# Performance work log

Hardware: AMD Instinct MI355X
Metric: run time of the kernel (lower is better)

## Reference

```python
import jax, jax.numpy as jnp
import numpy as np

N_NODES = 100000
N_EDGES = 400000
D_FEAT = 128
HIDDEN = 64
BETA = 1.0  # temperature default in concrete_sample


def setup_inputs() -> dict:
    key = jax.random.key(0)
    k = jax.random.split(key, 6)
    embed = jax.random.normal(k[0], (N_NODES, D_FEAT), dtype=jnp.float32)
    # elayers: Linear(4*F, 64) -> ReLU -> Linear(64, 1)
    W1 = jax.random.normal(k[1], (4 * D_FEAT, HIDDEN), dtype=jnp.float32) * (1.0 / np.sqrt(4 * D_FEAT))
    b1 = jnp.zeros((HIDDEN,), dtype=jnp.float32)
    W2 = jax.random.normal(k[2], (HIDDEN, 1), dtype=jnp.float32) * (1.0 / np.sqrt(HIDDEN))
    b2 = jnp.zeros((1,), dtype=jnp.float32)
    # per-edge uniform noise, as in torch.rand(w.size()); keep away from {0,1}
    noise = jax.random.uniform(k[3], (N_EDGES,), dtype=jnp.float32, minval=1e-6, maxval=1.0 - 1e-6)
    col = jax.random.randint(k[4], (N_EDGES,), 0, N_NODES, dtype=jnp.int64 if jax.config.jax_enable_x64 else jnp.int32)
    row = jax.random.randint(k[5], (N_EDGES,), 0, N_NODES, dtype=jnp.int64 if jax.config.jax_enable_x64 else jnp.int32)
    return {"embed": embed, "W1": W1, "b1": b1, "W2": W2, "b2": b2,
            "noise": noise, "col": col, "row": row, "src_idx": 0, "dst_idx": 1}


def reference(embed, W1, b1, W2, b2, noise, col, row, src_idx, dst_idx):
    E = col.shape[0]
    F = embed.shape[1]
    # gather per-edge endpoint embeddings + broadcast explained src/dst embeddings
    col_emb = embed[col]                                    # [E, F]
    row_emb = embed[row]                                    # [E, F]
    src_emb = jnp.broadcast_to(embed[src_idx], (E, F))       # [E, F]
    dst_emb = jnp.broadcast_to(embed[dst_idx], (E, F))       # [E, F]
    emb = jnp.concatenate([col_emb, row_emb, src_emb, dst_emb], axis=-1)  # [E, 4F]
    # elayers MLP
    h = jax.nn.relu(emb @ W1 + b1)                          # [E, 64]
    w = (h @ W2 + b2).reshape(-1)                           # [E]
    # concrete_sample (training=True, sample_bias=0): logit(noise) + w, sigmoid
    gate_inputs = (jnp.log(noise) - jnp.log1p(-noise) + w) / BETA
    values = jax.nn.sigmoid(gate_inputs)                    # [E] edge mask
    return values
```

## Files before the change

### kernel.cpp

```cpp
#include <hip/hip_runtime.h>
#include <hip/hip_bf16.h>


typedef __bf16 bf16x8 __attribute__((ext_vector_type(8)));
typedef float  f32x16 __attribute__((ext_vector_type(16)));
typedef unsigned short u16;

#define WSTR 264
#define Z16 {0.f,0.f,0.f,0.f,0.f,0.f,0.f,0.f,0.f,0.f,0.f,0.f,0.f,0.f,0.f,0.f}

__device__ __forceinline__ unsigned bfbits(float f){
  unsigned u = __builtin_bit_cast(unsigned, f);
  return (u + 0x7fffu + ((u >> 16) & 1u)) >> 16;
}
__device__ __forceinline__ unsigned pk2(float a, float b){
  return bfbits(a) | (bfbits(b) << 16);
}
__device__ __forceinline__ float bflo(unsigned u){ return __builtin_bit_cast(float, u << 16); }
__device__ __forceinline__ float bfhi(unsigned u){ return __builtin_bit_cast(float, u & 0xffff0000u); }

__global__ __launch_bounds__(256, 3) void fg_kernel(
    const float* __restrict__ embed, const float* __restrict__ W1,
    const float* __restrict__ b1, const int* __restrict__ srcp,
    const int* __restrict__ dstp, u16* __restrict__ F, u16* __restrict__ G, int NN)
{
  __shared__ __align__(16) u16 sW[64 * WSTR];
  __shared__ float sC[64];
  __shared__ float sRed[256];
  int tid = threadIdx.x;

  #pragma unroll
  for (int i = 0; i < 16; ++i){
    int idx = i * 256 + tid;
    int k = idx >> 4, q = idx & 15;
    float4 v = *(const float4*)(W1 + k * 64 + q * 4);
    sW[(4*q+0) * WSTR + k] = (u16)bfbits(v.x);
    sW[(4*q+1) * WSTR + k] = (u16)bfbits(v.y);
    sW[(4*q+2) * WSTR + k] = (u16)bfbits(v.z);
    sW[(4*q+3) * WSTR + k] = (u16)bfbits(v.w);
  }
  {
    int h = tid & 63, part = tid >> 6;
    int si = srcp[0], di = dstp[0];
    const float* se  = embed + (size_t)si * 128 + part * 32;
    const float* de  = embed + (size_t)di * 128 + part * 32;
    const float* w1s = W1 + (256 + part * 32) * 64 + h;
    const float* w1d = W1 + (384 + part * 32) * 64 + h;
    float acc = 0.f;
    #pragma unroll 8
    for (int k = 0; k < 32; ++k){
      acc += se[k] * w1s[k * 64];
      acc += de[k] * w1d[k * 64];
    }
    sRed[tid] = acc;
  }
  __syncthreads();
  if (tid < 64) sC[tid] = b1[tid] + sRed[tid] + sRed[64+tid] + sRed[128+tid] + sRed[192+tid];
  __syncthreads();

  int lane = tid & 63, wave = tid >> 6;
  int nl = lane & 31, h5 = lane >> 5;
  int tile = blockIdx.x * 128 + wave * 32;
  if (tile >= NN) return;
  const float* erow = embed + (size_t)(tile + nl) * 128;
  f32x16 aF0 = Z16, aF1 = Z16, aG0 = Z16, aG1 = Z16;
  const u16* sw0 = sW + nl * WSTR;
  const u16* sw1 = sW + (32 + nl) * WSTR;
  #pragma unroll
  for (int s = 0; s < 8; ++s){
    int ko = s * 16 + h5 * 8;
    float4 x = *(const float4*)(erow + ko);
    float4 y = *(const float4*)(erow + ko + 4);
    uint4 u; u.x = pk2(x.x,x.y); u.y = pk2(x.z,x.w); u.z = pk2(y.x,y.y); u.w = pk2(y.z,y.w);
    bf16x8 a = __builtin_bit_cast(bf16x8, u);
    bf16x8 bF0 = *(const bf16x8*)(sw0 + ko);
    bf16x8 bF1 = *(const bf16x8*)(sw1 + ko);
    bf16x8 bG0 = *(const bf16x8*)(sw0 + 128 + ko);
    bf16x8 bG1 = *(const bf16x8*)(sw1 + 128 + ko);
    aF0 = __builtin_amdgcn_mfma_f32_32x32x16_bf16(a, bF0, aF0, 0, 0, 0);
    aF1 = __builtin_amdgcn_mfma_f32_32x32x16_bf16(a, bF1, aF1, 0, 0, 0);
    aG0 = __builtin_amdgcn_mfma_f32_32x32x16_bf16(a, bG0, aG0, 0, 0, 0);
    aG1 = __builtin_amdgcn_mfma_f32_32x32x16_bf16(a, bG1, aG1, 0, 0, 0);
  }
  float cv0 = sC[nl], cv1 = sC[32 + nl];
  #pragma unroll
  for (int r = 0; r < 16; ++r){
    int node = tile + (r & 3) + 8 * (r >> 2) + 4 * h5;
    u16* fr = F + (size_t)node * 64 + nl;
    u16* gr = G + (size_t)node * 64 + nl;
    fr[0]  = (u16)bfbits(aF0[r] + cv0);
    fr[32] = (u16)bfbits(aF1[r] + cv1);
    gr[0]  = (u16)bfbits(aG0[r]);
    gr[32] = (u16)bfbits(aG1[r]);
  }
}

__global__ __launch_bounds__(256, 8) void edge_kernel(
    const u16* __restrict__ F, const u16* __restrict__ G,
    const float* __restrict__ W2, const float* __restrict__ b2,
    const float* __restrict__ noise, const int* __restrict__ col,
    const int* __restrict__ row, float* __restrict__ out, int E)
{
  int tid = threadIdx.x;
  int lane = tid & 63, wave = tid >> 6;
  int j = lane & 7, grp = lane >> 3;
  int e0 = blockIdx.x * 32 + wave * 8;
  if (e0 >= E) return;
  int e = e0 + grp; if (e >= E) e = E - 1;
  int ci = col[e], ri = row[e];
  uint4 fv = ((const uint4*)(F + (size_t)ci * 64))[j];
  uint4 gv = ((const uint4*)(G + (size_t)ri * 64))[j];
  float4 w2a = ((const float4*)W2)[2 * j];
  float4 w2b = ((const float4*)W2)[2 * j + 1];
  float p = 0.f, h;
  h = fmaxf(bflo(fv.x) + bflo(gv.x), 0.f); p += h * w2a.x;
  h = fmaxf(bfhi(fv.x) + bfhi(gv.x), 0.f); p += h * w2a.y;
  h = fmaxf(bflo(fv.y) + bflo(gv.y), 0.f); p += h * w2a.z;
  h = fmaxf(bfhi(fv.y) + bfhi(gv.y), 0.f); p += h * w2a.w;
  h = fmaxf(bflo(fv.z) + bflo(gv.z), 0.f); p += h * w2b.x;
  h = fmaxf(bfhi(fv.z) + bfhi(gv.z), 0.f); p += h * w2b.y;
  h = fmaxf(bflo(fv.w) + bflo(gv.w), 0.f); p += h * w2b.z;
  h = fmaxf(bfhi(fv.w) + bfhi(gv.w), 0.f); p += h * w2b.w;
  p += __shfl_xor(p, 1, 64);
  p += __shfl_xor(p, 2, 64);
  p += __shfl_xor(p, 4, 64);
  if (j == 0 && e0 + grp < E){
    float ns = noise[e];
    float g = logf(ns) - log1pf(-ns) + p + b2[0];
    out[e] = 1.f / (1.f + expf(-g));
  }
}

__global__ void naive_kernel(const float* __restrict__ embed, const float* __restrict__ W1,
    const float* __restrict__ b1, const float* __restrict__ W2, const float* __restrict__ b2,
    const float* __restrict__ noise, const int* __restrict__ col, const int* __restrict__ row,
    const int* __restrict__ srcp, const int* __restrict__ dstp, float* __restrict__ out, int E)
{
  int e = blockIdx.x * 256 + threadIdx.x;
  if (e >= E) return;
  int ci = col[e], ri = row[e], si = srcp[0], di = dstp[0];
  const float* ce = embed + (size_t)ci * 128;
  const float* re = embed + (size_t)ri * 128;
  const float* se = embed + (size_t)si * 128;
  const float* de = embed + (size_t)di * 128;
  float w = b2[0];
  for (int jj = 0; jj < 64; ++jj){
    float hh = b1[jj];
    for (int k = 0; k < 128; ++k){
      hh += ce[k] * W1[k * 64 + jj] + re[k] * W1[(128 + k) * 64 + jj]
          + se[k] * W1[(256 + k) * 64 + jj] + de[k] * W1[(384 + k) * 64 + jj];
    }
    w += fmaxf(hh, 0.f) * W2[jj];
  }
  float ns = noise[e];
  float g = logf(ns) - log1pf(-ns) + w;
  out[e] = 1.f / (1.f + expf(-g));
}

extern "C" void kernel_launch(void* const* d_in, const int* in_sizes, int n_in,
                              void* d_out, int out_size, void* d_ws, size_t ws_size,
                              hipStream_t stream)
{
  const float* embed = (const float*)d_in[0];
  const float* W1    = (const float*)d_in[1];
  const float* b1    = (const float*)d_in[2];
  const float* W2    = (const float*)d_in[3];
  const float* b2    = (const float*)d_in[4];
  const float* noise = (const float*)d_in[5];
  const int*   col   = (const int*)d_in[6];
  const int*   rowp  = (const int*)d_in[7];
  const int*   srcp  = (const int*)d_in[8];
  const int*   dstp  = (const int*)d_in[9];
  const int E  = in_sizes[5];
  const int NN = in_sizes[0] / 128;
  float* out = (float*)d_out;

  const size_t fBytes = (size_t)NN * 64 * sizeof(u16);
  if (ws_size >= 2 * fBytes){
    u16* F = (u16*)d_ws;
    u16* G = (u16*)((char*)d_ws + fBytes);
    fg_kernel<<<(NN + 127) / 128, 256, 0, stream>>>(embed, W1, b1, srcp, dstp, F, G, NN);
    edge_kernel<<<(E + 31) / 32, 256, 0, stream>>>(F, G, W2, b2, noise, col, rowp, out, E);
  } else {
    naive_kernel<<<(E + 255) / 256, 256, 0, stream>>>(embed, W1, b1, W2, b2, noise,
                                                      col, rowp, srcp, dstp, out, E);
  }
}
```

Baseline: 134.0 us.

## Fuse node projection and edge scoring into one cooperative persistent kernel

Merges the per-node projection kernel and the per-edge scoring kernel into a single persistent cooperative kernel, with a grid-wide sync between the two phases. Blocks loop over node tiles and then over edges, and each wave now handles two edges per iteration to raise memory-level parallelism. This removes one kernel launch and its gap. In exchange it adds grid-sync overhead, adds host-side occupancy queries on every call, and limits the edge phase to the occupancy chosen for the heavier projection kernel.

```diff
diff --git a/kernel.cpp b/kernel.cpp
--- a/kernel.cpp
+++ b/kernel.cpp
@@ -1,6 +1,9 @@
 #include <hip/hip_runtime.h>
 #include <hip/hip_bf16.h>
-
+#include <hip/hip_cooperative_groups.h>
+
+
+namespace cg = cooperative_groups;
 
 typedef __bf16 bf16x8 __attribute__((ext_vector_type(8)));
 typedef float  f32x16 __attribute__((ext_vector_type(16)));
@@ -19,15 +22,33 @@
 __device__ __forceinline__ float bflo(unsigned u){ return __builtin_bit_cast(float, u << 16); }
 __device__ __forceinline__ float bfhi(unsigned u){ return __builtin_bit_cast(float, u & 0xffff0000u); }
 
-__global__ __launch_bounds__(256, 3) void fg_kernel(
+__device__ __forceinline__ float edge_dot(uint4 fv, uint4 gv, float4 w2a, float4 w2b){
+  float p = 0.f, h;
+  h = fmaxf(bflo(fv.x) + bflo(gv.x), 0.f); p += h * w2a.x;
+  h = fmaxf(bfhi(fv.x) + bfhi(gv.x), 0.f); p += h * w2a.y;
+  h = fmaxf(bflo(fv.y) + bflo(gv.y), 0.f); p += h * w2a.z;
+  h = fmaxf(bfhi(fv.y) + bfhi(gv.y), 0.f); p += h * w2a.w;
+  h = fmaxf(bflo(fv.z) + bflo(gv.z), 0.f); p += h * w2b.x;
+  h = fmaxf(bfhi(fv.z) + bfhi(gv.z), 0.f); p += h * w2b.y;
+  h = fmaxf(bflo(fv.w) + bflo(gv.w), 0.f); p += h * w2b.z;
+  h = fmaxf(bfhi(fv.w) + bfhi(gv.w), 0.f); p += h * w2b.w;
+  return p;
+}
+
+__global__ __launch_bounds__(256, 3) void fused_kernel(
     const float* __restrict__ embed, const float* __restrict__ W1,
     const float* __restrict__ b1, const int* __restrict__ srcp,
-    const int* __restrict__ dstp, u16* __restrict__ F, u16* __restrict__ G, int NN)
+    const int* __restrict__ dstp, const float* __restrict__ W2,
+    const float* __restrict__ b2, const float* __restrict__ noise,
+    const int* __restrict__ col, const int* __restrict__ row,
+    u16* __restrict__ F, u16* __restrict__ G, float* __restrict__ out,
+    int NN, int E, int nBlocks)
 {
   __shared__ __align__(16) u16 sW[64 * WSTR];
   __shared__ float sC[64];
   __shared__ float sRed[256];
   int tid = threadIdx.x;
+  int lane = tid & 63, wave = tid >> 6;
 
   #pragma unroll
   for (int i = 0; i < 16; ++i){
@@ -58,76 +79,82 @@
   if (tid < 64) sC[tid] = b1[tid] + sRed[tid] + sRed[64+tid] + sRed[128+tid] + sRed[192+tid];
   __syncthreads();
 
-  int lane = tid & 63, wave = tid >> 6;
   int nl = lane & 31, h5 = lane >> 5;
-  int tile = blockIdx.x * 128 + wave * 32;
-  if (tile >= NN) return;
-  const float* erow = embed + (size_t)(tile + nl) * 128;
-  f32x16 aF0 = Z16, aF1 = Z16, aG0 = Z16, aG1 = Z16;
   const u16* sw0 = sW + nl * WSTR;
   const u16* sw1 = sW + (32 + nl) * WSTR;
-  #pragma unroll
-  for (int s = 0; s < 8; ++s){
-    int ko = s * 16 + h5 * 8;
-    float4 x = *(const float4*)(erow + ko);
-    float4 y = *(const float4*)(erow + ko + 4);
-    uint4 u; u.x = pk2(x.x,x.y); u.y = pk2(x.z,x.w); u.z = pk2(y.x,y.y); u.w = pk2(y.z,y.w);
-    bf16x8 a = __builtin_bit_cast(bf16x8, u);
-    bf16x8 bF0 = *(const bf16x8*)(sw0 + ko);
-    bf16x8 bF1 = *(const bf16x8*)(sw1 + ko);
-    bf16x8 bG0 = *(const bf16x8*)(sw0 + 128 + ko);
-    bf16x8 bG1 = *(const bf16x8*)(sw1 + 128 + ko);
-    aF0 = __builtin_amdgcn_mfma_f32_32x32x16_bf16(a, bF0, aF0, 0, 0, 0);
-    aF1 = __builtin_amdgcn_mfma_f32_32x32x16_bf16(a, bF1, aF1, 0, 0, 0);
-    aG0 = __builtin_amdgcn_mfma_f32_32x32x16_bf16(a, bG0, aG0, 0, 0, 0);
-    aG1 = __builtin_amdgcn_mfma_f32_32x32x16_bf16(a, bG1, aG1, 0, 0, 0);
-  }
   float cv0 = sC[nl], cv1 = sC[32 + nl];
-  #pragma unroll
-  for (int r = 0; r < 16; ++r){
-    int node = tile + (r & 3) + 8 * (r >> 2) + 4 * h5;
-    u16* fr = F + (size_t)node * 64 + nl;
-    u16* gr = G + (size_t)node * 64 + nl;
-    fr[0]  = (u16)bfbits(aF0[r] + cv0);
-    fr[32] = (u16)bfbits(aF1[r] + cv1);
-    gr[0]  = (u16)bfbits(aG0[r]);
-    gr[32] = (u16)bfbits(aG1[r]);
-  }
-}
-
-__global__ __launch_bounds__(256, 8) void edge_kernel(
-    const u16* __restrict__ F, const u16* __restrict__ G,
-    const float* __restrict__ W2, const float* __restrict__ b2,
-    const float* __restrict__ noise, const int* __restrict__ col,
-    const int* __restrict__ row, float* __restrict__ out, int E)
-{
-  int tid = threadIdx.x;
-  int lane = tid & 63, wave = tid >> 6;
+  for (int tile0 = blockIdx.x * 128; tile0 < NN; tile0 += nBlocks * 128){
+    int tile = tile0 + wave * 32;
+    if (tile < NN){
+      const float* erow = embed + (size_t)(tile + nl) * 128;
+      f32x16 aF0 = Z16, aF1 = Z16, aG0 = Z16, aG1 = Z16;
+      #pragma unroll
+      for (int s = 0; s < 8; ++s){
+        int ko = s * 16 + h5 * 8;
+        float4 x = *(const float4*)(erow + ko);
+        float4 y = *(const float4*)(erow + ko + 4);
+        uint4 u; u.x = pk2(x.x,x.y); u.y = pk2(x.z,x.w); u.z = pk2(y.x,y.y); u.w = pk2(y.z,y.w);
+        bf16x8 a = __builtin_bit_cast(bf16x8, u);
+        bf16x8 bF0 = *(const bf16x8*)(sw0 + ko);
+        bf16x8 bF1 = *(const bf16x8*)(sw1 + ko);
+        bf16x8 bG0 = *(const bf16x8*)(sw0 + 128 + ko);
+        bf16x8 bG1 = *(const bf16x8*)(sw1 + 128 + ko);
+        aF0 = __builtin_amdgcn_mfma_f32_32x32x16_bf16(a, bF0, aF0, 0, 0, 0);
+        aF1 = __builtin_amdgcn_mfma_f32_32x32x16_bf16(a, bF1, aF1, 0, 0, 0);
+        aG0 = __builtin_amdgcn_mfma_f32_32x32x16_bf16(a, bG0, aG0, 0, 0, 0);
+        aG1 = __builtin_amdgcn_mfma_f32_32x32x16_bf16(a, bG1, aG1, 0, 0, 0);
+      }
+      #pragma unroll
+      for (int r = 0; r < 16; ++r){
+        int node = tile + (r & 3) + 8 * (r >> 2) + 4 * h5;
+        u16* fr = F + (size_t)node * 64 + nl;
+        u16* gr = G + (size_t)node * 64 + nl;
+        fr[0]  = (u16)bfbits(aF0[r] + cv0);
+        fr[32] = (u16)bfbits(aF1[r] + cv1);
+        gr[0]  = (u16)bfbits(aG0[r]);
+        gr[32] = (u16)bfbits(aG1[r]);
+      }
+    }
+  }
+
+  __threadfence();
+  cg::this_grid().sync();
+  __threadfence();
+
   int j = lane & 7, grp = lane >> 3;
-  int e0 = blockIdx.x * 32 + wave * 8;
-  if (e0 >= E) return;
-  int e = e0 + grp; if (e >= E) e = E - 1;
-  int ci = col[e], ri = row[e];
-  uint4 fv = ((const uint4*)(F + (size_t)ci * 64))[j];
-  uint4 gv = ((const uint4*)(G + (size_t)ri * 64))[j];
   float4 w2a = ((const float4*)W2)[2 * j];
   float4 w2b = ((const float4*)W2)[2 * j + 1];
-  float p = 0.f, h;
-  h = fmaxf(bflo(fv.x) + bflo(gv.x), 0.f); p += h * w2a.x;
-  h = fmaxf(bfhi(fv.x) + bfhi(gv.x), 0.f); p += h * w2a.y;
-  h = fmaxf(bflo(fv.y) + bflo(gv.y), 0.f); p += h * w2a.z;
-  h = fmaxf(bfhi(fv.y) + bfhi(gv.y), 0.f); p += h * w2a.w;
-  h = fmaxf(bflo(fv.z) + bflo(gv.z), 0.f); p += h * w2b.x;
-  h = fmaxf(bfhi(fv.z) + bfhi(gv.z), 0.f); p += h * w2b.y;
-  h = fmaxf(bflo(fv.w) + bflo(gv.w), 0.f); p += h * w2b.z;
-  h = fmaxf(bfhi(fv.w) + bfhi(gv.w), 0.f); p += h * w2b.w;
-  p += __shfl_xor(p, 1, 64);
-  p += __shfl_xor(p, 2, 64);
-  p += __shfl_xor(p, 4, 64);
-  if (j == 0 && e0 + grp < E){
-    float ns = noise[e];
-    float g = logf(ns) - log1pf(-ns) + p + b2[0];
-    out[e] = 1.f / (1.f + expf(-g));
+  float b2v = b2[0];
+  int wgid = blockIdx.x * 4 + wave;
+  int stride = nBlocks * 4 * 16;
+  for (int base = wgid * 16; base < E; base += stride){
+    int eA = base + grp;
+    int eB = base + 8 + grp;
+    int eAc = eA < E ? eA : E - 1;
+    int eBc = eB < E ? eB : E - 1;
+    int ciA = col[eAc], riA = row[eAc];
+    int ciB = col[eBc], riB = row[eBc];
+    uint4 fvA = ((const uint4*)(F + (size_t)ciA * 64))[j];
+    uint4 gvA = ((const uint4*)(G + (size_t)riA * 64))[j];
+    uint4 fvB = ((const uint4*)(F + (size_t)ciB * 64))[j];
+    uint4 gvB = ((const uint4*)(G + (size_t)riB * 64))[j];
+    float pA = edge_dot(fvA, gvA, w2a, w2b);
+    float pB = edge_dot(fvB, gvB, w2a, w2b);
+    pA += __shfl_xor(pA, 1, 64); pB += __shfl_xor(pB, 1, 64);
+    pA += __shfl_xor(pA, 2, 64); pB += __shfl_xor(pB, 2, 64);
+    pA += __shfl_xor(pA, 4, 64); pB += __shfl_xor(pB, 4, 64);
+    if (j == 0){
+      if (eA < E){
+        float ns = noise[eA];
+        float g = logf(ns) - log1pf(-ns) + pA + b2v;
+        out[eA] = 1.f / (1.f + expf(-g));
+      }
+      if (eB < E){
+        float ns = noise[eB];
+        float g = logf(ns) - log1pf(-ns) + pB + b2v;
+        out[eB] = 1.f / (1.f + expf(-g));
+      }
+    }
   }
 }
 
@@ -171,16 +198,29 @@
   const int*   rowp  = (const int*)d_in[7];
   const int*   srcp  = (const int*)d_in[8];
   const int*   dstp  = (const int*)d_in[9];
-  const int E  = in_sizes[5];
-  const int NN = in_sizes[0] / 128;
+  int E  = in_sizes[5];
+  int NN = in_sizes[0] / 128;
   float* out = (float*)d_out;
 
   const size_t fBytes = (size_t)NN * 64 * sizeof(u16);
   if (ws_size >= 2 * fBytes){
     u16* F = (u16*)d_ws;
     u16* G = (u16*)((char*)d_ws + fBytes);
-    fg_kernel<<<(NN + 127) / 128, 256, 0, stream>>>(embed, W1, b1, srcp, dstp, F, G, NN);
-    edge_kernel<<<(E + 31) / 32, 256, 0, stream>>>(F, G, W2, b2, noise, col, rowp, out, E);
+    int dev = 0; hipGetDevice(&dev);
+    int nCU = 256;
+    hipDeviceGetAttribute(&nCU, hipDeviceAttributeMultiprocessorCount, dev);
+    int occ = 1;
+    hipOccupancyMaxActiveBlocksPerMultiprocessor(&occ, fused_kernel, 256, 0);
+    if (occ < 1) occ = 1;
+    int nBlocks = nCU * occ;
+    int maxUseful = (NN + 127) / 128;
+    if (nBlocks > maxUseful) nBlocks = maxUseful;
+    void* args[] = { (void*)&embed, (void*)&W1, (void*)&b1, (void*)&srcp, (void*)&dstp,
+                     (void*)&W2, (void*)&b2, (void*)&noise, (void*)&col, (void*)&rowp,
+                     (void*)&F, (void*)&G, (void*)&out, (void*)&NN, (void*)&E,
+                     (void*)&nBlocks };
+    hipLaunchCooperativeKernel((const void*)fused_kernel, dim3(nBlocks), dim3(256),
+                               args, 0, stream);
   } else {
     naive_kernel<<<(E + 255) / 256, 256, 0, stream>>>(embed, W1, b1, W2, b2, noise,
                                                       col, rowp, srcp, dstp, out, E);
```

Measured after the change: 315.2 us. 2.35x slower.

## Process one edge per thread in edge kernel and raise fg occupancy bound

Applied to the files above, without the earlier changes.

The edge kernel changes from eight lanes per edge with a shuffle reduction to one thread per edge. Each thread loads the full 128-byte F and G rows as eight uint4 loads each and accumulates the W2 dot product serially. This removes the cross-lane shuffles, gives coalesced col/row/noise/out accesses, and cuts the grid to one eighth the blocks. The trade is uncoalesced per-thread row gathers and higher register use. The fg_kernel launch bound is also raised from 3 to 4 waves-per-SIMD blocks.

```diff
diff --git a/kernel.cpp b/kernel.cpp
--- a/kernel.cpp
+++ b/kernel.cpp
@@ -19,7 +19,7 @@
 __device__ __forceinline__ float bflo(unsigned u){ return __builtin_bit_cast(float, u << 16); }
 __device__ __forceinline__ float bfhi(unsigned u){ return __builtin_bit_cast(float, u & 0xffff0000u); }
 
-__global__ __launch_bounds__(256, 3) void fg_kernel(
+__global__ __launch_bounds__(256, 4) void fg_kernel(
     const float* __restrict__ embed, const float* __restrict__ W1,
     const float* __restrict__ b1, const int* __restrict__ srcp,
     const int* __restrict__ dstp, u16* __restrict__ F, u16* __restrict__ G, int NN)
@@ -95,40 +95,41 @@
   }
 }
 
+__device__ __forceinline__ float acc8(uint4 fv, uint4 gv, const float* __restrict__ w2){
+  float p = 0.f, h;
+  h = fmaxf(bflo(fv.x) + bflo(gv.x), 0.f); p += h * w2[0];
+  h = fmaxf(bfhi(fv.x) + bfhi(gv.x), 0.f); p += h * w2[1];
+  h = fmaxf(bflo(fv.y) + bflo(gv.y), 0.f); p += h * w2[2];
+  h = fmaxf(bfhi(fv.y) + bfhi(gv.y), 0.f); p += h * w2[3];
+  h = fmaxf(bflo(fv.z) + bflo(gv.z), 0.f); p += h * w2[4];
+  h = fmaxf(bfhi(fv.z) + bfhi(gv.z), 0.f); p += h * w2[5];
+  h = fmaxf(bflo(fv.w) + bflo(gv.w), 0.f); p += h * w2[6];
+  h = fmaxf(bfhi(fv.w) + bfhi(gv.w), 0.f); p += h * w2[7];
+  return p;
+}
+
 __global__ __launch_bounds__(256, 8) void edge_kernel(
     const u16* __restrict__ F, const u16* __restrict__ G,
     const float* __restrict__ W2, const float* __restrict__ b2,
     const float* __restrict__ noise, const int* __restrict__ col,
     const int* __restrict__ row, float* __restrict__ out, int E)
 {
-  int tid = threadIdx.x;
-  int lane = tid & 63, wave = tid >> 6;
-  int j = lane & 7, grp = lane >> 3;
-  int e0 = blockIdx.x * 32 + wave * 8;
-  if (e0 >= E) return;
-  int e = e0 + grp; if (e >= E) e = E - 1;
+  int e = blockIdx.x * 256 + threadIdx.x;
+  if (e >= E) return;
   int ci = col[e], ri = row[e];
-  uint4 fv = ((const uint4*)(F + (size_t)ci * 64))[j];
-  uint4 gv = ((const uint4*)(G + (size_t)ri * 64))[j];
-  float4 w2a = ((const float4*)W2)[2 * j];
-  float4 w2b = ((const float4*)W2)[2 * j + 1];
-  float p = 0.f, h;
-  h = fmaxf(bflo(fv.x) + bflo(gv.x), 0.f); p += h * w2a.x;
-  h = fmaxf(bfhi(fv.x) + bfhi(gv.x), 0.f); p += h * w2a.y;
-  h = fmaxf(bflo(fv.y) + bflo(gv.y), 0.f); p += h * w2a.z;
-  h = fmaxf(bfhi(fv.y) + bfhi(gv.y), 0.f); p += h * w2a.w;
-  h = fmaxf(bflo(fv.z) + bflo(gv.z), 0.f); p += h * w2b.x;
-  h = fmaxf(bfhi(fv.z) + bfhi(gv.z), 0.f); p += h * w2b.y;
-  h = fmaxf(bflo(fv.w) + bflo(gv.w), 0.f); p += h * w2b.z;
-  h = fmaxf(bfhi(fv.w) + bfhi(gv.w), 0.f); p += h * w2b.w;
-  p += __shfl_xor(p, 1, 64);
-  p += __shfl_xor(p, 2, 64);
-  p += __shfl_xor(p, 4, 64);
-  if (j == 0 && e0 + grp < E){
-    float ns = noise[e];
-    float g = logf(ns) - log1pf(-ns) + p + b2[0];
-    out[e] = 1.f / (1.f + expf(-g));
-  }
+  float ns = noise[e];
+  const uint4* fp = (const uint4*)(F + (size_t)ci * 64);
+  const uint4* gp = (const uint4*)(G + (size_t)ri * 64);
+  uint4 f0 = fp[0], f1 = fp[1], f2 = fp[2], f3 = fp[3];
+  uint4 g0 = gp[0], g1 = gp[1], g2 = gp[2], g3 = gp[3];
+  float p = acc8(f0, g0, W2) + acc8(f1, g1, W2 + 8)
+          + acc8(f2, g2, W2 + 16) + acc8(f3, g3, W2 + 24);
+  uint4 f4 = fp[4], f5 = fp[5], f6 = fp[6], f7 = fp[7];
+  uint4 g4 = gp[4], g5 = gp[5], g6 = gp[6], g7 = gp[7];
+  p += acc8(f4, g4, W2 + 32) + acc8(f5, g5, W2 + 40)
+     + acc8(f6, g6, W2 + 48) + acc8(f7, g7, W2 + 56);
+  float g = logf(ns) - log1pf(-ns) + p + b2[0];
+  out[e] = 1.f / (1.f + expf(-g));
 }
 
 __global__ void naive_kernel(const float* __restrict__ embed, const float* __restrict__ W1,
@@ -180,7 +181,7 @@
     u16* F = (u16*)d_ws;
     u16* G = (u16*)((char*)d_ws + fBytes);
     fg_kernel<<<(NN + 127) / 128, 256, 0, stream>>>(embed, W1, b1, srcp, dstp, F, G, NN);
-    edge_kernel<<<(E + 31) / 32, 256, 0, stream>>>(F, G, W2, b2, noise, col, rowp, out, E);
+    edge_kernel<<<(E + 255) / 256, 256, 0, stream>>>(F, G, W2, b2, noise, col, rowp, out, E);
   } else {
     naive_kernel<<<(E + 255) / 256, 256, 0, stream>>>(embed, W1, b1, W2, b2, noise,
                                                       col, rowp, srcp, dstp, out, E);
```

Result: slower. 178.4 us (+33.2%).
